# Kernel optimization log

Hardware: AMD Instinct MI355X
Metric: run time of the kernel (lower is better)

Reference implementation:

```python
import jax, jax.numpy as jnp
import numpy as np

NUM_HEADS = 8
WINDOW = 33  # must be odd for seq length to be preserved


def setup_inputs() -> dict:
    key = jax.random.key(0)
    ks = jax.random.split(key, 7)
    B, S, E = 4, 2048, 256
    sc = 1.0 / np.sqrt(E)
    return {
        "x": jax.random.normal(ks[0], (B, S, E), dtype=jnp.float32),
        "Wq": jax.random.normal(ks[1], (E, E), dtype=jnp.float32) * sc,
        "bq": jax.random.normal(ks[2], (E,), dtype=jnp.float32) * 0.01,
        "Wk": jax.random.normal(ks[3], (E, E), dtype=jnp.float32) * sc,
        "bk": jax.random.normal(ks[4], (E,), dtype=jnp.float32) * 0.01,
        "Wv": jax.random.normal(ks[5], (E, E), dtype=jnp.float32) * sc,
        "bv": jax.random.normal(ks[6], (E,), dtype=jnp.float32) * 0.01,
    }


def reference(x, Wq, bq, Wk, bk, Wv, bv):
    B, S, E = x.shape
    H = NUM_HEADS
    D = E // H
    W = WINDOW
    pad = (W - 1) // 2
    scale = D ** (-0.5)

    def heads(t):  # [B,S,E] -> [B,H,S,D]
        return t.reshape(B, S, H, D).transpose(0, 2, 1, 3)

    q = heads(x @ Wq + bq)
    k = heads(x @ Wk + bk)
    v = heads(x @ Wv + bv)

    K = S - W + 1  # number of k/v windows (unfold with step=1)
    kv_idx = jnp.arange(K)[:, None] + jnp.arange(W)[None, :]  # [K,W]
    k_unf = k[:, :, kv_idx, :]  # [B,H,K,W,D]
    v_unf = v[:, :, kv_idx, :]  # [B,H,K,W,D]

    q_pad = jnp.pad(q, ((0, 0), (0, 0), (pad, pad), (0, 0)))  # zero pad seq
    q_idx = jnp.arange(S)[:, None] + jnp.arange(W)[None, :]  # [S,W]
    q_unf = q_pad[:, :, q_idx, :]  # [B,H,S,W,D]

    # contract over BOTH window and head dim (faithful to the torch einsums)
    scores = jnp.einsum('bhqwd,bhkwd->bhqk', q_unf, k_unf) * scale  # [B,H,S,K]
    attn = jax.nn.softmax(scores, axis=-1)
    out = jnp.einsum('bhqk,bhkwd->bhqd', attn, v_unf)  # sums v over window too
    return out.transpose(0, 2, 1, 3).reshape(B, S, E)
```

## Files before the change

### kernel.cpp

```cpp
#include <hip/hip_runtime.h>
#include <hip/hip_bf16.h>
#include <math.h>

#define BB   4
#define SS   2048
#define EE   256
#define HH   8
#define DD   32
#define WW   33
#define KKN  (SS - WW + 1)
#define SCALE 0.17677669529663687f
#define FMAX 20.0f
#define SCALE2 0.25503486f
#define FM2    28.853900817779268f

typedef __attribute__((ext_vector_type(8))) short short8v;
typedef __attribute__((ext_vector_type(4))) short short4v;
typedef __attribute__((ext_vector_type(4))) float float4v;

__device__ __forceinline__ short f2bf(float f) {
    union { __hip_bfloat16 h; short s; } c;
    c.h = __float2bfloat16(f);
    return c.s;
}

__device__ __forceinline__ short2 f2bf2(float a, float b) {
    union { __hip_bfloat162 h; short2 s; } c;
    float2 f; f.x = a; f.y = b;
    c.h = __float22bfloat162_rn(f);
    return c.s;
}

#if __has_builtin(__builtin_amdgcn_exp2f)
__device__ __forceinline__ float exp2_fast(float x) { return __builtin_amdgcn_exp2f(x); }
#else
__device__ __forceinline__ float exp2_fast(float x) { return __expf(x * 0.6931471805599453f); }
#endif

__global__ __launch_bounds__(256) void qkv_kernel(
    const float* __restrict__ x,
    const float* __restrict__ Wq, const float* __restrict__ bq,
    const float* __restrict__ Wk, const float* __restrict__ bk,
    const float* __restrict__ Wv, const float* __restrict__ bv,
    short* __restrict__ qo, short* __restrict__ ko, float* __restrict__ vo)
{
    __shared__ alignas(16) float xs[64][68];
    __shared__ alignas(16) float ws[64][68];

    const int t   = threadIdx.x;
    const int r0  = blockIdx.x * 64;
    const int ct  = blockIdx.y;
    const int mat = ct >> 2;
    const int cm0 = (ct & 3) * 64;
    const float* Wm   = (mat == 0) ? Wq : (mat == 1) ? Wk : Wv;
    const float* bias = (mat == 0) ? bq : (mat == 1) ? bk : bv;

    const int tr = t >> 4, tc = t & 15;

    float acc[4][4];
#pragma unroll
    for (int i = 0; i < 4; i++)
#pragma unroll
        for (int j = 0; j < 4; j++) acc[i][j] = 0.f;

    for (int ec = 0; ec < 4; ec++) {
        const int e0 = ec * 64;
        __syncthreads();
#pragma unroll
        for (int i = 0; i < 4; i++) {
            int L = t + i * 256;
            int r = L >> 4, c4 = (L & 15) * 4;
            *(float4*)&xs[r][c4] = *(const float4*)(x  + (size_t)(r0 + r) * EE + e0 + c4);
            *(float4*)&ws[r][c4] = *(const float4*)(Wm + (size_t)(e0 + r) * EE + cm0 + c4);
        }
        __syncthreads();

#pragma unroll
        for (int eg = 0; eg < 16; eg++) {
            float4 xv[4], wv4[4];
#pragma unroll
            for (int i = 0; i < 4; i++) xv[i]  = *(const float4*)&xs[tr * 4 + i][eg * 4];
#pragma unroll
            for (int j = 0; j < 4; j++) wv4[j] = *(const float4*)&ws[eg * 4 + j][tc * 4];
            const float* w0p = (const float*)&wv4[0];
            const float* w1p = (const float*)&wv4[1];
            const float* w2p = (const float*)&wv4[2];
            const float* w3p = (const float*)&wv4[3];
#pragma unroll
            for (int i = 0; i < 4; i++)
#pragma unroll
                for (int j = 0; j < 4; j++)
                    acc[i][j] = acc[i][j] + xv[i].x * w0p[j] + xv[i].y * w1p[j]
                                          + xv[i].z * w2p[j] + xv[i].w * w3p[j];
        }
    }

    const int cmb = cm0 + tc * 4;
    const int h = cmb >> 5, d0 = cmb & 31;
    float b4[4];
#pragma unroll
    for (int j = 0; j < 4; j++) b4[j] = bias[cmb + j];

#pragma unroll
    for (int i = 0; i < 4; i++) {
        int row = r0 + tr * 4 + i;
        int b_  = row >> 11;
        int s   = row & 2047;
        size_t o = (((size_t)(b_ * HH + h)) * SS + s) * DD + d0;
        if (mat == 2) {
            float4 vv;
            vv.x = acc[i][0] + b4[0]; vv.y = acc[i][1] + b4[1];
            vv.z = acc[i][2] + b4[2]; vv.w = acc[i][3] + b4[3];
            *(float4*)(vo + o) = vv;
        } else {
            short4v sv;
            sv.x = f2bf(acc[i][0] + b4[0]); sv.y = f2bf(acc[i][1] + b4[1]);
            sv.z = f2bf(acc[i][2] + b4[2]); sv.w = f2bf(acc[i][3] + b4[3]);
            *(short4v*)(((mat == 0) ? qo : ko) + o) = sv;
        }
    }
}

__global__ __launch_bounds__(64) void vs_kernel(
    const float* __restrict__ v, short* __restrict__ vsT)
{
    const int t   = threadIdx.x;
    const int d4  = t & 7;
    const int kkb = blockIdx.x * 8 + (t >> 3);
    const int bh  = blockIdx.y;
    if (kkb >= 252) return;
    const int kb0 = kkb * 8;

    const float4* vp = (const float4*)(v + ((size_t)bh * SS + kb0) * DD) + d4;
    float4 rbuf[7];
    float4 acc = {0.f, 0.f, 0.f, 0.f};
#pragma unroll
    for (int w = 0; w < WW; w++) {
        float4 xv = vp[w * 8];
        if (w < 7) rbuf[w] = xv;
        acc.x += xv.x; acc.y += xv.y; acc.z += xv.z; acc.w += xv.w;
    }
    short8v sh[4];
    sh[0][0] = f2bf(acc.x); sh[1][0] = f2bf(acc.y);
    sh[2][0] = f2bf(acc.z); sh[3][0] = f2bf(acc.w);
#pragma unroll
    for (int s = 1; s < 8; s++) {
        float4 sub = rbuf[s - 1];
        float4 add = vp[(s + 32) * 8];
        acc.x += add.x - sub.x; acc.y += add.y - sub.y;
        acc.z += add.z - sub.z; acc.w += add.w - sub.w;
        sh[0][s] = f2bf(acc.x); sh[1][s] = f2bf(acc.y);
        sh[2][s] = f2bf(acc.z); sh[3][s] = f2bf(acc.w);
    }
#pragma unroll
    for (int j = 0; j < 4; j++) {
        short* op = vsT + ((size_t)bh * DD + 4 * d4 + j) * KKN + kb0;
        *(short8v*)op = sh[j];
    }
}

__global__ __launch_bounds__(256, 4) void attn_kernel(
    const short* __restrict__ qg, const short* __restrict__ kg,
    const short* __restrict__ vsTg, float* __restrict__ out)
{
    __shared__ alignas(16) short QbS[64][40];
    __shared__ alignas(16) short Kb[128][40];
    __shared__ alignas(16) short Gst[96][72];
    __shared__ alignas(16) short vT[2][32][72];
    __shared__ float lrow[32];

    short (*Qb)[40] = QbS;
    short (*pb)[72] = (short (*)[72])QbS;

    const int t  = threadIdx.x;
    const int qt = blockIdx.x;
    const int bh = blockIdx.y;
    const int q0 = qt * 32;

    const short* qb   = qg   + (size_t)bh * SS * DD;
    const short* kb   = kg   + (size_t)bh * SS * DD;
    const short* vsTb = vsTg + (size_t)bh * DD * KKN;

    const int lane = t & 63, wv = t >> 6;
    const int quad = lane >> 4, lr = lane & 15;
    const int ptm = wv >> 1, ptn = wv & 1;
    const int jcol = 64 + (t & 7);

    const int qitw  = wv & 1;
    const int tbase = wv >> 1;
    const int qi    = qitw * 16 + lr;

    {
        short8v z = {0, 0, 0, 0, 0, 0, 0, 0};
        short* g = &Gst[0][0];
        for (int i = t; i < 864; i += 256) *(short8v*)(g + 8 * i) = z;
    }

    {
        int row = t >> 2, c8 = (t & 3) * 8;
        int gq = q0 - 16 + row;
        if (gq >= 0 && gq < SS) {
            *(short8v*)&Qb[row][c8] = *(const short8v*)(qb + (size_t)gq * DD + c8);
        } else {
            float4 z = {0.f, 0.f, 0.f, 0.f};
            *(float4*)&Qb[row][c8] = z;
        }
        *(short8v*)&Kb[row][c8]      = *(const short8v*)(kb + (size_t)row * DD + c8);
        *(short8v*)&Kb[64 + row][c8] = *(const short8v*)(kb + (size_t)(64 + row) * DD + c8);
    }
    if (t < 32) lrow[t] = 0.f;
    __syncthreads();

    short8v Qf[4];
#pragma unroll
    for (int tq = 0; tq < 4; tq++)
        Qf[tq] = *(const short8v*)&Qb[tq * 16 + lr][quad * 8];

    short8v Ufw[2];
#pragma unroll
    for (int ch = 0; ch < 2; ch++) {
        short8v u;
#pragma unroll
        for (int j = 0; j < 8; j++) {
            int m = ch * 32 + quad * 8 + j;
            u[j] = (qi <= m && m <= qi + 32) ? (short)0x3F80 : (short)0;
        }
        Ufw[ch] = u;
    }

    float4v acc = {0.f, 0.f, 0.f, 0.f};
    float lsumw = 0.f;
    const int npass = (wv < 2) ? 2 : 1;

    for (int kt = 0; kt < 32; kt++) {
        const int k0 = kt * 64;
        {
            int d_ = t >> 3, c8 = (t & 7) * 8;
            int col = k0 + c8; if (col > KKN - 8) col = KKN - 8;
            *(short8v*)&vT[kt & 1][d_][c8] =
                *(const short8v*)(vsTb + (size_t)d_ * KKN + col);
        }

        for (int pass = 0; pass < npass; pass++) {
            const int tk = wv + pass * 4;
            const int gr = k0 + tk * 16 + lr;
            const short8v A = *(const short8v*)&Kb[gr & 127][quad * 8];
#pragma unroll
            for (int tq = 0; tq < 4; tq++) {
                const int del = tk - tq;
                if (del < -2 || del > 4) continue;
                float4v c0 = {0.f, 0.f, 0.f, 0.f};
                c0 = __builtin_amdgcn_mfma_f32_16x16x32_bf16(A, Qf[tq], c0, 0, 0, 0);
                const int i   = tq * 16 + lr;
                const int j2b = tk * 16 + quad * 4 - i + 31;
                short* gbase = &Gst[0][i];
                short2 g01 = f2bf2(c0[0], c0[1]);
                short2 g23 = f2bf2(c0[2], c0[3]);
                short gv[4] = {g01.x, g01.y, g23.x, g23.y};
#pragma unroll
                for (int e = 0; e < 4; e++) {
                    int j2 = j2b + e;
                    short* dst = ((unsigned)j2 < 95u) ? (gbase + j2 * 72)
                                                      : (gbase + 95 * 72);
                    *dst = gv[e];
                }
            }
        }

        if (kt > 0) {
            const short8v Ap0 = *(const short8v*)&pb[ptm * 16 + lr][quad * 8];
            const short8v Ap1 = *(const short8v*)&pb[ptm * 16 + lr][32 + quad * 8];
            const short8v Bv0 = *(const short8v*)&vT[(kt - 1) & 1][ptn * 16 + lr][quad * 8];
            const short8v Bv1 = *(const short8v*)&vT[(kt - 1) & 1][ptn * 16 + lr][32 + quad * 8];
            __builtin_amdgcn_s_setprio(1);
            acc = __builtin_amdgcn_mfma_f32_16x16x32_bf16(Ap0, Bv0, acc, 0, 0, 0);
            acc = __builtin_amdgcn_mfma_f32_16x16x32_bf16(Ap1, Bv1, acc, 0, 0, 0);
            __builtin_amdgcn_s_setprio(0);
        }
        __syncthreads();

        if (kt < 31) {
            int r2 = t >> 2, c8 = (t & 3) * 8;
            int g  = k0 + 128 + r2;
            int ga = (g < SS) ? g : (SS - 1);
            *(short8v*)&Kb[g & 127][c8] = *(const short8v*)(kb + (size_t)ga * DD + c8);
        }

        const unsigned lim = (kt == 31) ? 32u : 64u;
        if (kt == 31) {
            short4v z4 = {0, 0, 0, 0};
            int zr = t >> 3, zc = (t & 7) * 4 + 32;
            *(short4v*)&pb[zr][zc] = z4;
        }

        short* prow = &pb[qi][0];
#pragma unroll
        for (int u = 0; u < 3; u++) {
            const int tile = 2 * u + tbase;
            const int jrow = tile * 16 + lr;
            const short8v A0f = *(const short8v*)&Gst[jrow][quad * 8];
            const short8v A1f = *(const short8v*)&Gst[jrow][32 + quad * 8];
            float4v D = {0.f, 0.f, 0.f, 0.f};
            __builtin_amdgcn_s_setprio(1);
            D = __builtin_amdgcn_mfma_f32_16x16x32_bf16(A0f, Ufw[0], D, 0, 0, 0);
            D = __builtin_amdgcn_mfma_f32_16x16x32_bf16(A1f, Ufw[1], D, 0, 0, 0);
            __builtin_amdgcn_s_setprio(0);
            const int kib = qi + tile * 16 + quad * 4 - 31;
            float p0 = exp2_fast(fmaf(D[0], SCALE2, -FM2));
            float p1 = exp2_fast(fmaf(D[1], SCALE2, -FM2));
            float p2 = exp2_fast(fmaf(D[2], SCALE2, -FM2));
            float p3 = exp2_fast(fmaf(D[3], SCALE2, -FM2));
            short2 c01 = f2bf2(p0, p1);
            short2 c23 = f2bf2(p2, p3);
            float pv[4] = {p0, p1, p2, p3};
            short cv[4] = {c01.x, c01.y, c23.x, c23.y};
#pragma unroll
            for (int e = 0; e < 4; e++) {
                int ki = kib + e;
                bool ok = (unsigned)ki < lim;
                short* dst = ok ? (prow + ki) : (prow + jcol);
                *dst = cv[e];
                lsumw += ok ? pv[e] : 0.f;
            }
        }
        __syncthreads();
    }

    {
        const short8v Ap0 = *(const short8v*)&pb[ptm * 16 + lr][quad * 8];
        const short8v Ap1 = *(const short8v*)&pb[ptm * 16 + lr][32 + quad * 8];
        const short8v Bv0 = *(const short8v*)&vT[1][ptn * 16 + lr][quad * 8];
        const short8v Bv1 = *(const short8v*)&vT[1][ptn * 16 + lr][32 + quad * 8];
        acc = __builtin_amdgcn_mfma_f32_16x16x32_bf16(Ap0, Bv0, acc, 0, 0, 0);
        acc = __builtin_amdgcn_mfma_f32_16x16x32_bf16(Ap1, Bv1, acc, 0, 0, 0);
    }

    {
        float s = lsumw;
        s += __shfl_xor(s, 16);
        s += __shfl_xor(s, 32);
        if (quad == 0) atomicAdd(&lrow[qitw * 16 + lr], s);
    }
    __syncthreads();

    {
        const int rrow = ptm * 16 + quad * 4;
        const int col  = ptn * 16 + lr;
        const int b_ = bh >> 3, h = bh & 7;
#pragma unroll
        for (int e = 0; e < 4; e++) {
            int s_ = q0 + rrow + e;
            out[((size_t)(b_ * SS + s_)) * EE + h * DD + col] = acc[e] / lrow[rrow + e];
        }
    }
}

extern "C" void kernel_launch(void* const* d_in, const int* in_sizes, int n_in,
                              void* d_out, int out_size, void* d_ws, size_t ws_size,
                              hipStream_t stream)
{
    (void)in_sizes; (void)n_in; (void)out_size; (void)ws_size;
    const float* x  = (const float*)d_in[0];
    const float* Wq = (const float*)d_in[1];
    const float* bq = (const float*)d_in[2];
    const float* Wk = (const float*)d_in[3];
    const float* bk = (const float*)d_in[4];
    const float* Wv = (const float*)d_in[5];
    const float* bv = (const float*)d_in[6];
    float* out = (float*)d_out;

    const size_t REG = (size_t)BB * HH * SS * DD;
    short* qbf   = (short*)d_ws;
    short* kbf   = qbf + REG;
    float* vbuf  = (float*)(kbf + REG);
    short* vsTb  = (short*)(vbuf + REG);

    qkv_kernel<<<dim3(128, 12), dim3(256), 0, stream>>>(x, Wq, bq, Wk, bk, Wv, bv,
                                                        qbf, kbf, vbuf);
    vs_kernel<<<dim3(32, 32), dim3(64), 0, stream>>>(vbuf, vsTb);
    attn_kernel<<<dim3(64, 32), dim3(256), 0, stream>>>(qbf, kbf, vsTb, out);
}
```

Before: 271.5 us.

## Shrink LDS ring buffers and stage global loads in registers to raise occupancy

Shrinks the K ring buffer from 128 to 96 rows and makes the V tile single-buffered. The next K and V tiles are now loaded into registers at the top of each iteration and written to LDS after the first barrier. Launch bounds are raised from 4 to 5 blocks per CU, so the smaller shared-memory footprint lets more blocks stay resident and global-load latency is hidden across the compute phase. In exchange it adds modulo-96 ring indexing and holds more values in registers, which may tighten the register budget under the higher occupancy target.

Result: slower. 618.8 us (+127.9%).

```diff
diff --git a/kernel.cpp b/kernel.cpp
--- a/kernel.cpp
+++ b/kernel.cpp
@@ -159,14 +159,14 @@
     }
 }
 
-__global__ __launch_bounds__(256, 4) void attn_kernel(
+__global__ __launch_bounds__(256, 5) void attn_kernel(
     const short* __restrict__ qg, const short* __restrict__ kg,
     const short* __restrict__ vsTg, float* __restrict__ out)
 {
     __shared__ alignas(16) short QbS[64][40];
-    __shared__ alignas(16) short Kb[128][40];
+    __shared__ alignas(16) short Kb[96][40];
     __shared__ alignas(16) short Gst[96][72];
-    __shared__ alignas(16) short vT[2][32][72];
+    __shared__ alignas(16) short vT[32][72];
     __shared__ float lrow[32];
 
     short (*Qb)[40] = QbS;
@@ -190,6 +190,9 @@
     const int tbase = wv >> 1;
     const int qi    = qitw * 16 + lr;
 
+    const int vd  = t >> 3, vc8 = (t & 7) * 8;
+    const int r2  = t >> 2, c8r = (t & 3) * 8;
+
     {
         short8v z = {0, 0, 0, 0, 0, 0, 0, 0};
         short* g = &Gst[0][0];
@@ -197,16 +200,16 @@
     }
 
     {
-        int row = t >> 2, c8 = (t & 3) * 8;
-        int gq = q0 - 16 + row;
+        int gq = q0 - 16 + r2;
         if (gq >= 0 && gq < SS) {
-            *(short8v*)&Qb[row][c8] = *(const short8v*)(qb + (size_t)gq * DD + c8);
+            *(short8v*)&Qb[r2][c8r] = *(const short8v*)(qb + (size_t)gq * DD + c8r);
         } else {
             float4 z = {0.f, 0.f, 0.f, 0.f};
-            *(float4*)&Qb[row][c8] = z;
-        }
-        *(short8v*)&Kb[row][c8]      = *(const short8v*)(kb + (size_t)row * DD + c8);
-        *(short8v*)&Kb[64 + row][c8] = *(const short8v*)(kb + (size_t)(64 + row) * DD + c8);
+            *(float4*)&Qb[r2][c8r] = z;
+        }
+        *(short8v*)&Kb[r2][c8r] = *(const short8v*)(kb + (size_t)r2 * DD + c8r);
+        if (t < 128)
+            *(short8v*)&Kb[64 + r2][c8r] = *(const short8v*)(kb + (size_t)(64 + r2) * DD + c8r);
     }
     if (t < 32) lrow[t] = 0.f;
     __syncthreads();
@@ -231,20 +234,26 @@
     float4v acc = {0.f, 0.f, 0.f, 0.f};
     float lsumw = 0.f;
     const int npass = (wv < 2) ? 2 : 1;
+    int k0m = 0;
 
     for (int kt = 0; kt < 32; kt++) {
         const int k0 = kt * 64;
+        short8v vstage;
         {
-            int d_ = t >> 3, c8 = (t & 7) * 8;
-            int col = k0 + c8; if (col > KKN - 8) col = KKN - 8;
-            *(short8v*)&vT[kt & 1][d_][c8] =
-                *(const short8v*)(vsTb + (size_t)d_ * KKN + col);
+            int col = k0 + vc8; if (col > KKN - 8) col = KKN - 8;
+            vstage = *(const short8v*)(vsTb + (size_t)vd * KKN + col);
+        }
+        short8v kstage;
+        if (kt < 31) {
+            int gp = k0 + 96 + r2;
+            int ga = (gp < SS) ? gp : (SS - 1);
+            kstage = *(const short8v*)(kb + (size_t)ga * DD + c8r);
         }
 
         for (int pass = 0; pass < npass; pass++) {
             const int tk = wv + pass * 4;
-            const int gr = k0 + tk * 16 + lr;
-            const short8v A = *(const short8v*)&Kb[gr & 127][quad * 8];
+            int krow = k0m + tk * 16 + lr; if (krow >= 96) krow -= 96;
+            const short8v A = *(const short8v*)&Kb[krow][quad * 8];
 #pragma unroll
             for (int tq = 0; tq < 4; tq++) {
                 const int del = tk - tq;
@@ -270,8 +279,8 @@
         if (kt > 0) {
             const short8v Ap0 = *(const short8v*)&pb[ptm * 16 + lr][quad * 8];
             const short8v Ap1 = *(const short8v*)&pb[ptm * 16 + lr][32 + quad * 8];
-            const short8v Bv0 = *(const short8v*)&vT[(kt - 1) & 1][ptn * 16 + lr][quad * 8];
-            const short8v Bv1 = *(const short8v*)&vT[(kt - 1) & 1][ptn * 16 + lr][32 + quad * 8];
+            const short8v Bv0 = *(const short8v*)&vT[ptn * 16 + lr][quad * 8];
+            const short8v Bv1 = *(const short8v*)&vT[ptn * 16 + lr][32 + quad * 8];
             __builtin_amdgcn_s_setprio(1);
             acc = __builtin_amdgcn_mfma_f32_16x16x32_bf16(Ap0, Bv0, acc, 0, 0, 0);
             acc = __builtin_amdgcn_mfma_f32_16x16x32_bf16(Ap1, Bv1, acc, 0, 0, 0);
@@ -279,11 +288,10 @@
         }
         __syncthreads();
 
+        *(short8v*)&vT[vd][vc8] = vstage;
         if (kt < 31) {
-            int r2 = t >> 2, c8 = (t & 3) * 8;
-            int g  = k0 + 128 + r2;
-            int ga = (g < SS) ? g : (SS - 1);
-            *(short8v*)&Kb[g & 127][c8] = *(const short8v*)(kb + (size_t)ga * DD + c8);
+            int slot = k0m + r2; if (slot >= 96) slot -= 96;
+            *(short8v*)&Kb[slot][c8r] = kstage;
         }
 
         const unsigned lim = (kt == 31) ? 32u : 64u;
@@ -324,13 +332,14 @@
             }
         }
         __syncthreads();
+        k0m += 64; if (k0m >= 96) k0m -= 96;
     }
 
     {
         const short8v Ap0 = *(const short8v*)&pb[ptm * 16 + lr][quad * 8];
         const short8v Ap1 = *(const short8v*)&pb[ptm * 16 + lr][32 + quad * 8];
-        const short8v Bv0 = *(const short8v*)&vT[1][ptn * 16 + lr][quad * 8];
-        const short8v Bv1 = *(const short8v*)&vT[1][ptn * 16 + lr][32 + quad * 8];
+        const short8v Bv0 = *(const short8v*)&vT[ptn * 16 + lr][quad * 8];
+        const short8v Bv1 = *(const short8v*)&vT[ptn * 16 + lr][32 + quad * 8];
         acc = __builtin_amdgcn_mfma_f32_16x16x32_bf16(Ap0, Bv0, acc, 0, 0, 0);
         acc = __builtin_amdgcn_mfma_f32_16x16x32_bf16(Ap1, Bv1, acc, 0, 0, 0);
     }
```
